# Kernel tuning notes

Hardware: AMD Instinct MI355X
Metric: run time of the kernel (lower is better)

Reference implementation:

```python
import jax, jax.numpy as jnp
import numpy as np

HEADS = 4
DIM_HEAD = 32


def setup_inputs() -> dict:
    key = jax.random.key(0)
    k1, k2, k3, k4 = jax.random.split(key, 4)
    b, dim, t = 8, 64, 16384
    inner = HEADS * DIM_HEAD  # 128
    x = jax.random.normal(k1, (b, dim, t), dtype=jnp.float32)
    # Conv1d(dim, inner*3, kernel=1, bias=False) -> weight (3*inner, dim)
    w_qkv = jax.random.normal(k2, (3 * inner, dim), dtype=jnp.float32) * (1.0 / np.sqrt(dim))
    # Conv1d(inner, dim, kernel=1) -> weight (dim, inner), bias (dim,)
    w_out = jax.random.normal(k3, (dim, inner), dtype=jnp.float32) * (1.0 / np.sqrt(inner))
    b_out = jax.random.normal(k4, (dim,), dtype=jnp.float32) * 0.01
    return {"x": x, "w_qkv": w_qkv, "w_out": w_out, "b_out": b_out}


def reference(x, w_qkv, w_out, b_out):
    b, c, t = x.shape
    h, dh = HEADS, DIM_HEAD
    # 1x1 conv == per-timestep matmul: (b, 3*inner, t)
    qkv = jnp.einsum('oc,bct->bot', w_qkv, x)
    q, k, v = jnp.split(qkv, 3, axis=1)
    q = q.reshape(b, h, dh, t)
    k = k.reshape(b, h, dh, t)
    v = v.reshape(b, h, dh, t)
    q = jax.nn.softmax(q, axis=-1)   # softmax over time
    k = jax.nn.softmax(k, axis=-2)   # softmax over head-dim d
    # einsum('bhdt,bhds->bhds', k, v): sums k over t, broadcast-scales v
    context = jnp.einsum('bhdt,bhds->bhds', k, v)
    # einsum('bhdt,bhds->bhdt', q, context): sums context over s, scales q
    out = jnp.einsum('bhdt,bhds->bhdt', q, context)
    out = out.reshape(b, h * dh, t)
    # to_out 1x1 conv with bias
    return jnp.einsum('oc,bct->bot', w_out, out) + b_out[None, :, None]
```

## Files before the change

kernel.cpp:

```cpp
#include <hip/hip_runtime.h>
#include <math.h>


typedef short short8 __attribute__((ext_vector_type(8)));
typedef short short4s __attribute__((ext_vector_type(4)));
typedef float f32x4 __attribute__((ext_vector_type(4)));

namespace {
constexpr int NB = 8;
constexpr int NC = 64;
constexpr int NT = 16384;
constexpr int NI = 128;
constexpr int TBK = 256;
constexpr int CPB = NT / TBK;
constexpr int NBLK = NB * CPB;
constexpr int XSP = 72;
constexpr int PTP = 136;
constexpr int PT  = 32;
constexpr int REP = 8;

constexpr int WS_ZQ   = 0;
constexpr int WS_KSUM = WS_ZQ + REP * NB * NI;
constexpr int WS_XSUM = WS_KSUM + REP * NB * NI;
constexpr int WS_NFLOAT = WS_XSUM + REP * NB * NC;
}

__device__ __forceinline__ unsigned short f2bf(float f) {
  unsigned u = __float_as_uint(f);
  u += 0x7fffu + ((u >> 16) & 1u);
  return (unsigned short)(u >> 16);
}

template <bool XS>
__device__ __forceinline__ void stage_x(const float* __restrict__ xb, int t0,
                                        unsigned short* xs, float* xsum_dst, int tid) {
  const int c = tid >> 2, tq = tid & 3;
  const float4* xr = (const float4*)(xb + (size_t)c * NT + t0);
  float s = 0.f;
#pragma unroll 4
  for (int i = 0; i < 16; ++i) {
    const int tv = tq + 4 * i;
    float4 v = xr[tv];
    if (XS) s += (v.x + v.y) + (v.z + v.w);
    const int t = 4 * tv;
    xs[(t + 0) * XSP + c] = f2bf(v.x);
    xs[(t + 1) * XSP + c] = f2bf(v.y);
    xs[(t + 2) * XSP + c] = f2bf(v.z);
    xs[(t + 3) * XSP + c] = f2bf(v.w);
  }
  if (XS) {
    s += __shfl_xor(s, 1, 64);
    s += __shfl_xor(s, 2, 64);
    if (tq == 0) atomicAdd(xsum_dst + c, s);
  }
}

__device__ __forceinline__ void load_aq(const float* __restrict__ wqkv, int w,
                                        int lm, int quad, short8 aq[2][2]) {
#pragma unroll
  for (int tile = 0; tile < 2; ++tile)
#pragma unroll
    for (int s = 0; s < 2; ++s) {
      const float* pq = wqkv + (size_t)(32 * w + tile * 16 + lm) * NC + s * 32 + quad * 8;
#pragma unroll
      for (int j = 0; j < 8; ++j) aq[tile][s][j] = (short)f2bf(pq[j]);
    }
}

__global__ __launch_bounds__(256) void la_stats(
    const float* __restrict__ x, const float* __restrict__ wqkv,
    float* __restrict__ ws)
{
  __shared__ __align__(16) unsigned short xs[TBK * XSP];

  const int bid = blockIdx.x;
  const int b = bid >> 6, chunk = bid & 63;
  const int rep = chunk & (REP - 1);
  const int tid = threadIdx.x, lane = tid & 63;
  const int w = __builtin_amdgcn_readfirstlane(tid >> 6);
  const int lm = lane & 15, quad = lane >> 4;
  const float* xb = x + (size_t)b * NC * NT;

  stage_x<true>(xb, chunk * TBK, xs, ws + WS_XSUM + (rep * NB + b) * NC, tid);

  short8 aq[2][2], ak[2][2];
  load_aq(wqkv, w, lm, quad, aq);
#pragma unroll
  for (int tile = 0; tile < 2; ++tile)
#pragma unroll
    for (int s = 0; s < 2; ++s) {
      const float* pk = wqkv + (size_t)(NI + 32 * w + tile * 16 + lm) * NC + s * 32 + quad * 8;
#pragma unroll
      for (int j = 0; j < 8; ++j) ak[tile][s][j] = (short)f2bf(pk[j]);
    }

  float zq_acc[2][4] = {};
  float ks_acc[2][4] = {};
  __syncthreads();

  for (int tc = 0; tc < TBK / 16; ++tc) {
    short8 bf[2];
#pragma unroll
    for (int s = 0; s < 2; ++s)
      bf[s] = *(const short8*)&xs[(tc * 16 + lm) * XSP + s * 32 + quad * 8];
    f32x4 cq[2] = {{0,0,0,0},{0,0,0,0}}, ck[2] = {{0,0,0,0},{0,0,0,0}};
#pragma unroll
    for (int tile = 0; tile < 2; ++tile)
#pragma unroll
      for (int s = 0; s < 2; ++s) {
        cq[tile] = __builtin_amdgcn_mfma_f32_16x16x32_bf16(aq[tile][s], bf[s], cq[tile], 0, 0, 0);
        ck[tile] = __builtin_amdgcn_mfma_f32_16x16x32_bf16(ak[tile][s], bf[s], ck[tile], 0, 0, 0);
      }
    float ke[2][4];
    float zt = 0.f;
#pragma unroll
    for (int tile = 0; tile < 2; ++tile)
#pragma unroll
      for (int r = 0; r < 4; ++r) {
        zq_acc[tile][r] += __expf(cq[tile][r]);
        float e = __expf(ck[tile][r]);
        ke[tile][r] = e;
        zt += e;
      }
    zt += __shfl_xor(zt, 16, 64);
    zt += __shfl_xor(zt, 32, 64);
    const float rz = __builtin_amdgcn_rcpf(zt);
#pragma unroll
    for (int tile = 0; tile < 2; ++tile)
#pragma unroll
      for (int r = 0; r < 4; ++r)
        ks_acc[tile][r] = fmaf(ke[tile][r], rz, ks_acc[tile][r]);
  }

#pragma unroll
  for (int tile = 0; tile < 2; ++tile)
#pragma unroll
    for (int r = 0; r < 4; ++r) {
      float a = zq_acc[tile][r], k = ks_acc[tile][r];
#pragma unroll
      for (int off = 1; off < 16; off <<= 1) {
        a += __shfl_xor(a, off, 64);
        k += __shfl_xor(k, off, 64);
      }
      if (lm == 0) {
        const int c = 32 * w + tile * 16 + quad * 4 + r;
        atomicAdd(ws + WS_ZQ + (rep * NB + b) * NI + c, a);
        atomicAdd(ws + WS_KSUM + (rep * NB + b) * NI + c, k);
      }
    }
}

__global__ __launch_bounds__(256) void la_out(
    const float* __restrict__ x, const float* __restrict__ wqkv,
    const float* __restrict__ wout, const float* __restrict__ bout,
    const float* __restrict__ ws, float* __restrict__ y)
{
  __shared__ __align__(16) unsigned short xs[TBK * XSP];
  __shared__ __align__(16) unsigned short pt[PT * PTP];
  __shared__ float scale_s[NI];
  __shared__ float xsum_s[NC];

  const int bid = blockIdx.x;
  const int b = bid >> 6, chunk = bid & 63;
  const int tid = threadIdx.x, lane = tid & 63;
  const int w = __builtin_amdgcn_readfirstlane(tid >> 6);
  const int lm = lane & 15, quad = lane >> 4;
  const int t0 = chunk * TBK;
  const float* xb = x + (size_t)b * NC * NT;

  stage_x<false>(xb, t0, xs, nullptr, tid);

  if (tid < NC) {
    float s = 0.f;
#pragma unroll
    for (int rp = 0; rp < REP; ++rp) s += ws[WS_XSUM + (rp * NB + b) * NC + tid];
    xsum_s[tid] = s;
  }
  __syncthreads();
  if (tid < NI) {
    float vs = 0.f;
    const float* wv = wqkv + (size_t)(2 * NI + tid) * NC;
#pragma unroll 8
    for (int cc = 0; cc < NC; ++cc) vs = fmaf(wv[cc], xsum_s[cc], vs);
    float zq_t = 0.f, ks_t = 0.f;
#pragma unroll
    for (int rp = 0; rp < REP; ++rp) {
      zq_t += ws[WS_ZQ + (rp * NB + b) * NI + tid];
      ks_t += ws[WS_KSUM + (rp * NB + b) * NI + tid];
    }
    scale_s[tid] = ks_t * vs / zq_t;
  }
  __syncthreads();

  short8 aq[2][2];
  load_aq(wqkv, w, lm, quad, aq);
  short8 aw[4];
  {
    const int o = 16 * w + lm;
#pragma unroll
    for (int s = 0; s < 4; ++s) {
      const float* wo = wout + (size_t)o * NI + s * 32 + quad * 8;
#pragma unroll
      for (int j = 0; j < 8; ++j)
        aw[s][j] = (short)f2bf(wo[j] * scale_s[s * 32 + quad * 8 + j]);
    }
  }
  float bias[4];
#pragma unroll
  for (int r = 0; r < 4; ++r) bias[r] = bout[16 * w + quad * 4 + r];

  for (int sub = 0; sub < TBK / PT; ++sub) {
    for (int tc = 0; tc < PT / 16; ++tc) {
      const int tl = sub * PT + tc * 16;
      short8 bf[2];
#pragma unroll
      for (int s = 0; s < 2; ++s)
        bf[s] = *(const short8*)&xs[(tl + lm) * XSP + s * 32 + quad * 8];
      f32x4 cq[2] = {{0,0,0,0},{0,0,0,0}};
#pragma unroll
      for (int tile = 0; tile < 2; ++tile)
#pragma unroll
        for (int s = 0; s < 2; ++s)
          cq[tile] = __builtin_amdgcn_mfma_f32_16x16x32_bf16(aq[tile][s], bf[s], cq[tile], 0, 0, 0);
#pragma unroll
      for (int tile = 0; tile < 2; ++tile) {
        short4s pv;
#pragma unroll
        for (int r = 0; r < 4; ++r) pv[r] = (short)f2bf(__expf(cq[tile][r]));
        *(short4s*)&pt[(tc * 16 + lm) * PTP + 32 * w + tile * 16 + quad * 4] = pv;
      }
    }
    __syncthreads();
    for (int tc = 0; tc < PT / 16; ++tc) {
      short8 bp[4];
#pragma unroll
      for (int s = 0; s < 4; ++s)
        bp[s] = *(const short8*)&pt[(tc * 16 + lm) * PTP + s * 32 + quad * 8];
      f32x4 acc = {bias[0], bias[1], bias[2], bias[3]};
#pragma unroll
      for (int s = 0; s < 4; ++s)
        acc = __builtin_amdgcn_mfma_f32_16x16x32_bf16(aw[s], bp[s], acc, 0, 0, 0);
#pragma unroll
      for (int r = 0; r < 4; ++r)
        y[((size_t)b * NC + 16 * w + quad * 4 + r) * NT + t0 + sub * PT + tc * 16 + lm] = acc[r];
    }
    __syncthreads();
  }
}

extern "C" void kernel_launch(void* const* d_in, const int* in_sizes, int n_in,
                              void* d_out, int out_size, void* d_ws, size_t ws_size,
                              hipStream_t stream)
{
  const float* x    = (const float*)d_in[0];
  const float* wqkv = (const float*)d_in[1];
  const float* wout = (const float*)d_in[2];
  const float* bout = (const float*)d_in[3];
  float* y  = (float*)d_out;
  float* ws = (float*)d_ws;

  if (ws_size < (size_t)WS_NFLOAT * sizeof(float)) return;

  hipMemsetAsync(ws, 0, (size_t)WS_NFLOAT * sizeof(float), stream);
  la_stats<<<dim3(NBLK), 256, 0, stream>>>(x, wqkv, ws);
  la_out<<<dim3(NBLK), 256, 0, stream>>>(x, wqkv, wout, bout, ws, y);
}
```

Measured before the change: 114.6 us.

## Fuse stats and output kernels into one cooperative kernel with grid sync

Merges the statistics pass and the output pass into a single cooperative kernel separated by a grid-wide barrier. The staged bf16 x tile and the q weights stay in LDS and registers across the barrier, so x is read from global memory once instead of twice and one launch is removed. In exchange, all 512 blocks must be co-resident (launch bounds set to 2 blocks per SM), the cooperative launch and grid sync add their own cost, and the launch fails if residency cannot be met.

Measured after the change: 216.7 us. 1.89x slower.

```diff
diff --git a/kernel.cpp b/kernel.cpp
--- a/kernel.cpp
+++ b/kernel.cpp
@@ -1,5 +1,8 @@
 #include <hip/hip_runtime.h>
+#include <hip/hip_cooperative_groups.h>
 #include <math.h>
+
+namespace cg = cooperative_groups;
 
 
 typedef short short8 __attribute__((ext_vector_type(8)));
@@ -67,11 +70,15 @@
     }
 }
 
-__global__ __launch_bounds__(256) void la_stats(
+__global__ __launch_bounds__(256, 2) void la_fused(
     const float* __restrict__ x, const float* __restrict__ wqkv,
-    float* __restrict__ ws)
+    const float* __restrict__ wout, const float* __restrict__ bout,
+    float* __restrict__ ws, float* __restrict__ y)
 {
   __shared__ __align__(16) unsigned short xs[TBK * XSP];
+  __shared__ __align__(16) unsigned short pt[PT * PTP];
+  __shared__ float scale_s[NI];
+  __shared__ float xsum_s[NC];
 
   const int bid = blockIdx.x;
   const int b = bid >> 6, chunk = bid & 63;
@@ -79,9 +86,10 @@
   const int tid = threadIdx.x, lane = tid & 63;
   const int w = __builtin_amdgcn_readfirstlane(tid >> 6);
   const int lm = lane & 15, quad = lane >> 4;
+  const int t0 = chunk * TBK;
   const float* xb = x + (size_t)b * NC * NT;
 
-  stage_x<true>(xb, chunk * TBK, xs, ws + WS_XSUM + (rep * NB + b) * NC, tid);
+  stage_x<true>(xb, t0, xs, ws + WS_XSUM + (rep * NB + b) * NC, tid);
 
   short8 aq[2][2], ak[2][2];
   load_aq(wqkv, w, lm, quad, aq);
@@ -148,32 +156,15 @@
         atomicAdd(ws + WS_KSUM + (rep * NB + b) * NI + c, k);
       }
     }
-}
-
-__global__ __launch_bounds__(256) void la_out(
-    const float* __restrict__ x, const float* __restrict__ wqkv,
-    const float* __restrict__ wout, const float* __restrict__ bout,
-    const float* __restrict__ ws, float* __restrict__ y)
-{
-  __shared__ __align__(16) unsigned short xs[TBK * XSP];
-  __shared__ __align__(16) unsigned short pt[PT * PTP];
-  __shared__ float scale_s[NI];
-  __shared__ float xsum_s[NC];
-
-  const int bid = blockIdx.x;
-  const int b = bid >> 6, chunk = bid & 63;
-  const int tid = threadIdx.x, lane = tid & 63;
-  const int w = __builtin_amdgcn_readfirstlane(tid >> 6);
-  const int lm = lane & 15, quad = lane >> 4;
-  const int t0 = chunk * TBK;
-  const float* xb = x + (size_t)b * NC * NT;
-
-  stage_x<false>(xb, t0, xs, nullptr, tid);
-
+
+  __threadfence();
+  cg::this_grid().sync();
+
+  const volatile float* vws = ws;
   if (tid < NC) {
     float s = 0.f;
 #pragma unroll
-    for (int rp = 0; rp < REP; ++rp) s += ws[WS_XSUM + (rp * NB + b) * NC + tid];
+    for (int rp = 0; rp < REP; ++rp) s += vws[WS_XSUM + (rp * NB + b) * NC + tid];
     xsum_s[tid] = s;
   }
   __syncthreads();
@@ -185,15 +176,13 @@
     float zq_t = 0.f, ks_t = 0.f;
 #pragma unroll
     for (int rp = 0; rp < REP; ++rp) {
-      zq_t += ws[WS_ZQ + (rp * NB + b) * NI + tid];
-      ks_t += ws[WS_KSUM + (rp * NB + b) * NI + tid];
+      zq_t += vws[WS_ZQ + (rp * NB + b) * NI + tid];
+      ks_t += vws[WS_KSUM + (rp * NB + b) * NI + tid];
     }
     scale_s[tid] = ks_t * vs / zq_t;
   }
   __syncthreads();
 
-  short8 aq[2][2];
-  load_aq(wqkv, w, lm, quad, aq);
   short8 aw[4];
   {
     const int o = 16 * w + lm;
@@ -262,6 +251,8 @@
   if (ws_size < (size_t)WS_NFLOAT * sizeof(float)) return;
 
   hipMemsetAsync(ws, 0, (size_t)WS_NFLOAT * sizeof(float), stream);
-  la_stats<<<dim3(NBLK), 256, 0, stream>>>(x, wqkv, ws);
-  la_out<<<dim3(NBLK), 256, 0, stream>>>(x, wqkv, wout, bout, ws, y);
-}
+  void* args[] = { (void*)&x, (void*)&wqkv, (void*)&wout, (void*)&bout,
+                   (void*)&ws, (void*)&y };
+  hipLaunchCooperativeKernel(reinterpret_cast<void*>(la_fused), dim3(NBLK),
+                             dim3(256), args, 0, stream);
+}
```
